# Performance work log

Hardware: AMD Instinct MI355X
Metric: run time of the kernel (lower is better)

Reference implementation:

```python
import jax, jax.numpy as jnp
import numpy as np

N_NEIGHBORS = 15
N_BATCHES = 3
TEMPERATURE = 1.0
DISTANCE_MASK_SENTINEL = 1e10  # pushes self-distance out of the neighborhood
EPS = 1e-8


def setup_inputs() -> dict:
    key = jax.random.key(0)
    k1, k2 = jax.random.split(key)
    embeddings = jax.random.normal(k1, (8192, 512), dtype=jnp.float32)
    batch_labels = jax.random.randint(k2, (8192,), 0, N_BATCHES, dtype=jnp.int32)
    return {"embeddings": embeddings, "batch_labels": batch_labels}


def reference(embeddings, batch_labels):
    n_cells = embeddings.shape[0]
    # pairwise squared euclidean distances: [n, n]
    sq_norms = jnp.sum(embeddings ** 2, axis=-1)
    distances = sq_norms[:, None] + sq_norms[None, :] - 2.0 * (embeddings @ embeddings.T)
    distances = distances + jnp.eye(n_cells, dtype=distances.dtype) * DISTANCE_MASK_SENTINEL

    # soft neighbor weights
    neighbor_weights = jax.nn.softmax(-distances / TEMPERATURE, axis=-1)

    # differentiable sort along rows (jnp.sort is piecewise-linear, differentiable)
    sorted_dists = jnp.sort(distances, axis=-1)
    kth_dist = sorted_dists[:, N_NEIGHBORS - 1:N_NEIGHBORS]  # [n, 1]

    # soft less(distances, kth_dist): sigmoid((kth - d) / softness)
    k_mask = jax.nn.sigmoid((kth_dist - distances) / TEMPERATURE)

    neighbor_weights = neighbor_weights * k_mask
    neighbor_weights = neighbor_weights / (neighbor_weights.sum(axis=-1, keepdims=True) + EPS)

    # batch distribution in each soft neighborhood: [n, n_batches]
    batch_onehot = jax.nn.one_hot(batch_labels, N_BATCHES, dtype=neighbor_weights.dtype)
    batch_dist = neighbor_weights @ batch_onehot

    per_cell_entropy = -jnp.sum(batch_dist * jnp.log(batch_dist + EPS), axis=-1)
    max_entropy = jnp.log(jnp.asarray(N_BATCHES, dtype=jnp.float32))
    normalized_entropy = per_cell_entropy / (max_entropy + EPS)
    return -jnp.mean(normalized_entropy)
```

## Files before the change

### kernel.cpp

```cpp
#include <hip/hip_runtime.h>
#include <math.h>

#define N_CELLS 8192
#define DIM 512
#define TILE 128
#define BK 64
#define KITERS (DIM / BK)
#define NSTRIPE (N_CELLS / TILE)
#define NTRI (NSTRIPE * (NSTRIPE + 1) / 2)
#define SAMPLE 512
#define CAP 512
#define WQCAP 1024

typedef float f32x4 __attribute__((ext_vector_type(4)));
typedef _Float16 f16x8 __attribute__((ext_vector_type(8)));

#define AS1U(p) ((const __attribute__((address_space(1))) unsigned int*)(p))
#define AS3U(p) ((__attribute__((address_space(3))) unsigned int*)(p))

__device__ __forceinline__ unsigned fkey(float f) {
    unsigned u = __float_as_uint(f);
    return (u & 0x80000000u) ? ~u : (u | 0x80000000u);
}
__device__ __forceinline__ float finv(unsigned k) {
    unsigned u = (k & 0x80000000u) ? (k ^ 0x80000000u) : ~k;
    return __uint_as_float(u);
}

__global__ __launch_bounds__(256) void prep_kernel(const float* __restrict__ E,
                                                   unsigned short* __restrict__ Efp,
                                                   float* __restrict__ norms,
                                                   float* __restrict__ out) {
    if (blockIdx.x == 0 && threadIdx.x == 0) out[0] = 0.0f;
    const int wave = threadIdx.x >> 6, lane = threadIdx.x & 63;
    const int row = blockIdx.x * 4 + wave;
    const float4* e4 = (const float4*)(E + (size_t)row * DIM);
    float4 a = e4[lane * 2], b = e4[lane * 2 + 1];
    f16x8 h;
    h[0] = (_Float16)a.x; h[1] = (_Float16)a.y; h[2] = (_Float16)a.z; h[3] = (_Float16)a.w;
    h[4] = (_Float16)b.x; h[5] = (_Float16)b.y; h[6] = (_Float16)b.z; h[7] = (_Float16)b.w;
    const int kc = lane >> 3;
    const int u  = lane & 7;
    *(f16x8*)(Efp + ((size_t)kc * N_CELLS + row) * 64 + (size_t)(u ^ (row & 7)) * 8) = h;
    float s = a.x*a.x + a.y*a.y + a.z*a.z + a.w*a.w
            + b.x*b.x + b.y*b.y + b.z*b.z + b.w*b.w;
    #pragma unroll
    for (int off = 32; off > 0; off >>= 1) s += __shfl_down(s, off, 64);
    if (lane == 0) norms[row] = s;
}

__global__ __launch_bounds__(256) void norms_kernel(const float* __restrict__ E,
                                                    float* __restrict__ norms,
                                                    float* __restrict__ out) {
    if (blockIdx.x == 0 && threadIdx.x == 0) out[0] = 0.0f;
    const int wave = threadIdx.x >> 6, lane = threadIdx.x & 63;
    const int row = blockIdx.x * 4 + wave;
    const float4* e4 = (const float4*)(E + (size_t)row * DIM);
    float4 a = e4[lane], b = e4[lane + 64];
    float s = a.x*a.x + a.y*a.y + a.z*a.z + a.w*a.w
            + b.x*b.x + b.y*b.y + b.z*b.z + b.w*b.w;
    #pragma unroll
    for (int off = 32; off > 0; off >>= 1) s += __shfl_down(s, off, 64);
    if (lane == 0) norms[row] = s;
}


#define STAGE_PACKED(BUF, it)                                                                     \
    do {                                                                                          \
        const unsigned short* pa_ = Efp + ((size_t)(it) * N_CELLS + arow) * 64;                   \
        const unsigned short* pb_ = Efp + ((size_t)(it) * N_CELLS + brow) * 64;                   \
        _Pragma("unroll")                                                                         \
        for (int q_ = 0; q_ < 4; q_++) {                                                          \
            __builtin_amdgcn_global_load_lds(AS1U(pa_ + q_*2048 + t*8),                           \
                                             AS3U((BUF) + q_*4096 + t*16), 16, 0, 0);             \
            __builtin_amdgcn_global_load_lds(AS1U(pb_ + q_*2048 + t*8),                           \
                                             AS3U((BUF) + 16384 + q_*4096 + t*16), 16, 0, 0);     \
        }                                                                                         \
    } while (0)

#define GEMM_COMPUTE(BUF)                                                                         \
    do {                                                                                          \
        _Pragma("unroll")                                                                         \
        for (int ks = 0; ks < 2; ks++) {                                                          \
            f16x8 af[4], bf[4];                                                                   \
            _Pragma("unroll")                                                                     \
            for (int tm = 0; tm < 4; tm++)                                                        \
                af[tm] = *(const f16x8*)((BUF) + (size_t)(wr*64 + tm*16 + fr) * 128               \
                                              + (((ks*4 + kg) * 16) ^ fx));                       \
            _Pragma("unroll")                                                                     \
            for (int tn = 0; tn < 4; tn++)                                                        \
                bf[tn] = *(const f16x8*)((BUF) + 16384 + (size_t)(wc*64 + tn*16 + fr) * 128       \
                                              + (((ks*4 + kg) * 16) ^ fx));                       \
            _Pragma("unroll")                                                                     \
            for (int tm = 0; tm < 4; tm++)                                                        \
                _Pragma("unroll")                                                                 \
                for (int tn = 0; tn < 4; tn++)                                                    \
                    acc[tm][tn] = __builtin_amdgcn_mfma_f32_16x16x32_f16(af[tm], bf[tn],          \
                                                                         acc[tm][tn], 0, 0, 0);  \
        }                                                                                         \
    } while (0)

#define GEMM_LOOP()                                                                               \
    do {                                                                                          \
        _Pragma("unroll")                                                                         \
        for (int it2 = 0; it2 < KITERS; it2 += 2) {                                               \
            __syncthreads();                                                                      \
            STAGE_PACKED(smem, it2);                                                              \
            STAGE_PACKED(smem + 32768, it2 + 1);                                                  \
            __syncthreads();                                                                      \
            GEMM_COMPUTE(smem);                                                                   \
            GEMM_COMPUTE(smem + 32768);                                                           \
        }                                                                                         \
        __syncthreads();                                                                          \
    } while (0)

__global__ __launch_bounds__(256) void samp_dist_kernel(const unsigned short* __restrict__ Efp,
                                                        const float* __restrict__ norms,
                                                        float* __restrict__ Dsamp) {
    __shared__ __align__(16) char smem[65536];

    const int t = threadIdx.x;
    const int lane = t & 63;
    const int w = t >> 6;
    const int wr = w >> 1, wc = w & 1;

    const int arow = blockIdx.y * TILE;
    const int brow = blockIdx.x * TILE;

    const int kg = lane >> 4;
    const int fr = lane & 15;
    const int fx = (fr & 7) << 4;

    f32x4 acc[4][4];
    #pragma unroll
    for (int a = 0; a < 4; a++)
        #pragma unroll
        for (int b = 0; b < 4; b++)
            acc[a][b] = (f32x4){0.f, 0.f, 0.f, 0.f};

    GEMM_LOOP();

    const int colb = brow + wc * 64 + fr;
    const int rowb = arow + wr * 64 + (lane >> 4) * 4;
    #pragma unroll
    for (int tn = 0; tn < 4; tn++) {
        const int col = colb + tn * 16;
        const float nj = norms[col];
        #pragma unroll
        for (int tm = 0; tm < 4; tm++) {
            #pragma unroll
            for (int r = 0; r < 4; r++) {
                const int row = rowb + tm * 16 + r;
                float d = norms[row] + nj - 2.0f * acc[tm][tn][r];
                if (row == col) d += 1e10f;
                Dsamp[(size_t)row * SAMPLE + col] = d;
            }
        }
    }
}

__global__ __launch_bounds__(256) void tsel_kernel(const float* __restrict__ Dsamp,
                                                   float* __restrict__ T,
                                                   int* __restrict__ cnt) {
    const int row = blockIdx.x * 4 + (threadIdx.x >> 6);
    const int lane = threadIdx.x & 63;
    const float4* r4 = (const float4*)(Dsamp + (size_t)row * SAMPLE);

    float v[8];
    #pragma unroll
    for (int s = 0; s < 2; s++) {
        float4 d4 = r4[s * 64 + lane];
        v[s*4+0] = d4.x; v[s*4+1] = d4.y; v[s*4+2] = d4.z; v[s*4+3] = d4.w;
    }
    float mn = v[0], mx = v[0];
    #pragma unroll
    for (int k = 1; k < 8; k++) { mn = fminf(mn, v[k]); mx = fmaxf(mx, v[k]); }
    #pragma unroll
    for (int off = 32; off > 0; off >>= 1) {
        mn = fminf(mn, __shfl_down(mn, off, 64));
        mx = fmaxf(mx, __shfl_down(mx, off, 64));
    }
    mn = __shfl(mn, 0, 64);
    mx = __shfl(mx, 0, 64);

    unsigned lo = fkey(mn), hi = fkey(mx);
    int it = 0;
    while (lo < hi && it < 34) {
        it++;
        const unsigned mid = lo + ((hi - lo) >> 1);
        const float fm = finv(mid);
        int c = 0;
        #pragma unroll
        for (int k = 0; k < 8; k++) c += (v[k] <= fm) ? 1 : 0;
        #pragma unroll
        for (int off = 32; off > 0; off >>= 1) c += __shfl_down(c, off, 64);
        c = __shfl(c, 0, 64);
        if (c >= 15) hi = mid; else lo = mid + 1;
    }
    if (lane == 0) { T[row] = finv(lo); cnt[row] = 0; }
}

__global__ __launch_bounds__(256) void main_cand_kernel(const unsigned short* __restrict__ Efp,
                                                        const float* __restrict__ norms,
                                                        const int* __restrict__ labels,
                                                        const float* __restrict__ T,
                                                        int* __restrict__ cnt,
                                                        int2* __restrict__ cand) {
    __shared__ __align__(16) char smem[65536];

    const int t = threadIdx.x;
    const int lane = t & 63;
    const int w = t >> 6;
    const int wr = w >> 1, wc = w & 1;

    const int fid = blockIdx.x;
    const int y = fid / 65;
    const int x = fid - y * 65;
    const int a = (x <= y) ? y : (NSTRIPE - 1 - y);
    const int b = (x <= y) ? x : (x - y - 1);

    const int arow = a * TILE;
    const int brow = b * TILE;
    const bool diag = (a == b);

    const int kg = lane >> 4;
    const int fr = lane & 15;
    const int fx = (fr & 7) << 4;

    f32x4 acc[4][4];
    #pragma unroll
    for (int aa = 0; aa < 4; aa++)
        #pragma unroll
        for (int bb = 0; bb < 4; bb++)
            acc[aa][bb] = (f32x4){0.f, 0.f, 0.f, 0.f};

    GEMM_LOOP();

    int2* wq = (int2*)(smem + (size_t)w * 8192);

    const int colb = brow + wc * 64 + fr;
    const int rowb = arow + wr * 64 + (lane >> 4) * 4;

    float Trow[4][4], Nrow[4][4];
    int Lrow[4][4];
    #pragma unroll
    for (int tm = 0; tm < 4; tm++)
        #pragma unroll
        for (int r = 0; r < 4; r++) {
            const int row = rowb + tm * 16 + r;
            Trow[tm][r] = T[row];
            Nrow[tm][r] = norms[row];
            Lrow[tm][r] = labels[row];
        }
    float Tcol[4];
    #pragma unroll
    for (int tn = 0; tn < 4; tn++) Tcol[tn] = T[colb + tn * 16];

    int wn = 0;
    #pragma unroll
    for (int tn = 0; tn < 4; tn++) {
        const int col = colb + tn * 16;
        const float nj = norms[col];
        const int labc = labels[col];
        #pragma unroll
        for (int tm = 0; tm < 4; tm++) {
            #pragma unroll
            for (int r = 0; r < 4; r++) {
                const int row = rowb + tm * 16 + r;
                const float d = Nrow[tm][r] + nj - 2.0f * acc[tm][tn][r];
                const bool live = !diag || (row > col);
                {
                    const bool hit = live && (d <= Trow[tm][r]);
                    const unsigned long long bal = __ballot(hit);
                    if (hit) {
                        const int pos = __popcll(bal & ((1ull << lane) - 1ull));
                        if (wn + pos < WQCAP)
                            wq[wn + pos] = make_int2(__float_as_int(d), row | (labc << 13));
                    }
                    wn += (int)__popcll(bal);
                }
                {
                    const bool hit = live && (d <= Tcol[tn]);
                    const unsigned long long bal = __ballot(hit);
                    if (hit) {
                        const int pos = __popcll(bal & ((1ull << lane) - 1ull));
                        if (wn + pos < WQCAP)
                            wq[wn + pos] = make_int2(__float_as_int(d), col | (Lrow[tm][r] << 13));
                    }
                    wn += (int)__popcll(bal);
                }
            }
        }
    }

    const int qn = (wn < WQCAP) ? wn : WQCAP;
    for (int i = lane; i < qn; i += 64) {
        const int2 e = wq[i];
        const int row = e.y & 8191;
        const int lab = e.y >> 13;
        const int idx = atomicAdd(&cnt[row], 1);
        if (idx < CAP) cand[(size_t)row * CAP + idx] = make_int2(e.x, lab);
    }
    if (wn > WQCAP)
        for (int r2 = lane; r2 < TILE; r2 += 64) {
            atomicAdd(&cnt[arow + r2], 1000000);
            atomicAdd(&cnt[brow + r2], 1000000);
        }
}

__global__ __launch_bounds__(256) void final_kernel(const int2* __restrict__ cand,
                                                    const int* __restrict__ cnt,
                                                    const float* __restrict__ T,
                                                    float* __restrict__ rowloss) {
    const int row = blockIdx.x * 4 + (threadIdx.x >> 6);
    const int lane = threadIdx.x & 63;
    const int n = cnt[row];
    if (n < 15 || n > CAP) return;

    float d[CAP / 64];
    int lb[CAP / 64];
    #pragma unroll
    for (int s = 0; s < CAP / 64; s++) {
        const int idx = s * 64 + lane;
        if (idx < n) {
            const int2 c = cand[(size_t)row * CAP + idx];
            d[s] = __int_as_float(c.x);
            lb[s] = c.y;
        } else { d[s] = 3.0e38f; lb[s] = 3; }
    }

    float dmin = d[0];
    #pragma unroll
    for (int s = 1; s < CAP / 64; s++) dmin = fminf(dmin, d[s]);
    #pragma unroll
    for (int off = 32; off > 0; off >>= 1) dmin = fminf(dmin, __shfl_down(dmin, off, 64));
    dmin = __shfl(dmin, 0, 64);

    unsigned lo = fkey(dmin), hi = fkey(T[row]);
    int it = 0;
    while (lo < hi && it < 34) {
        it++;
        const unsigned mid = lo + ((hi - lo) >> 1);
        const float fm = finv(mid);
        int c = 0;
        #pragma unroll
        for (int s = 0; s < CAP / 64; s++) c += (d[s] <= fm) ? 1 : 0;
        #pragma unroll
        for (int off = 32; off > 0; off >>= 1) c += __shfl_down(c, off, 64);
        c = __shfl(c, 0, 64);
        if (c >= 15) hi = mid; else lo = mid + 1;
    }
    const float kth = finv(lo);

    float z = 0.f, s0 = 0.f, s1 = 0.f, s2 = 0.f;
    #pragma unroll
    for (int s = 0; s < CAP / 64; s++) {
        const float w = __expf(dmin - d[s]);
        const float msk = 1.0f / (1.0f + __expf(d[s] - kth));
        const float p = w * msk;
        z  += w;
        s0 += (lb[s] == 0) ? p : 0.f;
        s1 += (lb[s] == 1) ? p : 0.f;
        s2 += (lb[s] == 2) ? p : 0.f;
    }
    #pragma unroll
    for (int off = 32; off > 0; off >>= 1) {
        z  += __shfl_down(z,  off, 64);
        s0 += __shfl_down(s0, off, 64);
        s1 += __shfl_down(s1, off, 64);
        s2 += __shfl_down(s2, off, 64);
    }
    if (lane == 0) {
        const float ssum = s0 + s1 + s2;
        const float denom = ssum + 1e-8f * z;
        const float q0 = s0/denom, q1 = s1/denom, q2 = s2/denom;
        const float H = -(q0*logf(q0+1e-8f) + q1*logf(q1+1e-8f) + q2*logf(q2+1e-8f));
        rowloss[row] = -(H / (logf(3.0f) + 1e-8f)) * (1.0f / N_CELLS);
    }
}

__global__ __launch_bounds__(512) void reduce_kernel(const float* __restrict__ rowloss,
                                                     float* __restrict__ out) {
    __shared__ float wsum[8];
    const int t = threadIdx.x, lane = t & 63, wv = t >> 6;
    const float4* r4 = (const float4*)rowloss;
    float s = 0.f;
    for (int i = t; i < N_CELLS / 4; i += 512) {
        const float4 v = r4[i];
        s += v.x + v.y + v.z + v.w;
    }
    #pragma unroll
    for (int off = 32; off > 0; off >>= 1) s += __shfl_down(s, off, 64);
    if (lane == 0) wsum[wv] = s;
    __syncthreads();
    if (t == 0) {
        float tot = 0.f;
        #pragma unroll
        for (int i = 0; i < 8; i++) tot += wsum[i];
        out[0] = tot;
    }
}

template<int NT>
__device__ __forceinline__ void finish_row(const float* rowb,
                                           float lst[15],
                                           const int* __restrict__ labels,
                                           float* __restrict__ out,
                                           float* __restrict__ rowloss,
                                           int rowidx) {
    constexpr int WAVES = NT / 64;
    __shared__ float w0s[WAVES], w14s[WAVES];
    __shared__ int cnt;
    __shared__ float zz[WAVES], r0s[WAVES], r1s[WAVES], r2s[WAVES];

    const int t = threadIdx.x;
    const int lane = t & 63, wave = t >> 6;

    float m0 = lst[0], m14 = lst[14];
    #pragma unroll
    for (int off = 32; off > 0; off >>= 1) {
        m0  = fminf(m0,  __shfl_down(m0,  off, 64));
        m14 = fminf(m14, __shfl_down(m14, off, 64));
    }
    if (lane == 0) { w0s[wave] = m0; w14s[wave] = m14; }
    __syncthreads();
    float dmin = w0s[0], ub = w14s[0];
    #pragma unroll
    for (int i = 1; i < WAVES; i++) { dmin = fminf(dmin, w0s[i]); ub = fminf(ub, w14s[i]); }

    unsigned lo = fkey(dmin), hi = fkey(ub);
    int iter = 0;
    while (lo < hi && iter < 34) {
        iter++;
        const unsigned mid = lo + ((hi - lo) >> 1);
        const float fmid = finv(mid);
        int c = 0;
        #pragma unroll
        for (int k = 0; k < 15; k++) c += (lst[k] <= fmid) ? 1 : 0;
        #pragma unroll
        for (int off = 32; off > 0; off >>= 1) c += __shfl_down(c, off, 64);
        __syncthreads();
        if (t == 0) cnt = 0;
        __syncthreads();
        if (lane == 0) atomicAdd(&cnt, c);
        __syncthreads();
        const int total = cnt;
        if (total >= 15) hi = mid; else lo = mid + 1;
    }
    const float kth = finv(hi);

    const float4* rb4 = (const float4*)rowb;
    const int4* lb4 = (const int4*)labels;
    float z = 0.f, s0 = 0.f, s1 = 0.f, s2 = 0.f;
    #pragma unroll
    for (int s = 0; s < N_CELLS / (4 * NT); s++) {
        const int idx = s * NT + t;
        const float4 d4 = rb4[idx];
        const int4 l4 = lb4[idx];
        #pragma unroll
        for (int c2 = 0; c2 < 4; c2++) {
            const float d = (c2 == 0) ? d4.x : (c2 == 1) ? d4.y : (c2 == 2) ? d4.z : d4.w;
            const int lab = (c2 == 0) ? l4.x : (c2 == 1) ? l4.y : (c2 == 2) ? l4.z : l4.w;
            const float w = __expf(dmin - d);
            const float msk = 1.0f / (1.0f + __expf(d - kth));
            const float p = w * msk;
            z  += w;
            s0 += (lab == 0) ? p : 0.f;
            s1 += (lab == 1) ? p : 0.f;
            s2 += (lab == 2) ? p : 0.f;
        }
    }
    #pragma unroll
    for (int off = 32; off > 0; off >>= 1) {
        z  += __shfl_down(z,  off, 64);
        s0 += __shfl_down(s0, off, 64);
        s1 += __shfl_down(s1, off, 64);
        s2 += __shfl_down(s2, off, 64);
    }
    if (lane == 0) { zz[wave] = z; r0s[wave] = s0; r1s[wave] = s1; r2s[wave] = s2; }
    __syncthreads();
    if (t == 0) {
        float Z = 0.f, S0 = 0.f, S1 = 0.f, S2 = 0.f;
        #pragma unroll
        for (int i = 0; i < WAVES; i++) { Z += zz[i]; S0 += r0s[i]; S1 += r1s[i]; S2 += r2s[i]; }
        const float ssum = S0 + S1 + S2;
        const float denom = ssum + 1e-8f * Z;
        const float q0 = S0/denom, q1 = S1/denom, q2 = S2/denom;
        const float H = -(q0*logf(q0+1e-8f) + q1*logf(q1+1e-8f) + q2*logf(q2+1e-8f));
        const float contrib = -(H / (logf(3.0f) + 1e-8f)) * (1.0f / N_CELLS);
        if (rowloss) rowloss[rowidx] = contrib;
        else atomicAdd(out, contrib);
    }
}

__device__ void process_row(int i,
                            const float* __restrict__ E,
                            const float* __restrict__ norms,
                            const int* __restrict__ labels,
                            float* __restrict__ out,
                            float* __restrict__ rowloss,
                            float* rowb, float* ei) {
    const int t = threadIdx.x;
    __syncthreads();
    for (int k = t; k < DIM; k += 512) ei[k] = E[(size_t)i * DIM + k];
    __syncthreads();
    const float ni = norms[i];

    float lst[15];
    #pragma unroll
    for (int k = 0; k < 15; k++) lst[k] = 3.0e38f;

    for (int s = 0; s < N_CELLS / 512; s++) {
        const int j = s * 512 + t;
        const float* ej = E + (size_t)j * DIM;
        float dot = 0.f;
        #pragma unroll 4
        for (int k = 0; k < DIM; k += 4) {
            float4 e4 = *(const float4*)(ej + k);
            dot += ei[k]*e4.x + ei[k+1]*e4.y + ei[k+2]*e4.z + ei[k+3]*e4.w;
        }
        float d = ni + norms[j] - 2.0f * dot;
        if (j == i) d += 1e10f;
        rowb[j] = d;
        float v = d;
        #pragma unroll
        for (int k = 0; k < 15; k++) {
            float lo2 = fminf(lst[k], v);
            v = fmaxf(lst[k], v);
            lst[k] = lo2;
        }
    }
    finish_row<512>(rowb, lst, labels, out, rowloss, i);
}

__global__ __launch_bounds__(512) void fused_kernel(const float* __restrict__ E,
                                                    const float* __restrict__ norms,
                                                    const int* __restrict__ labels,
                                                    float* __restrict__ out,
                                                    float* __restrict__ rowloss,
                                                    const int* __restrict__ cnt_g) {
    __shared__ float rowb[N_CELLS];
    __shared__ float ei[DIM];
    __shared__ int bad[TILE];
    __shared__ int nbad;
    const int t = threadIdx.x;

    if (cnt_g == nullptr) {
        process_row(blockIdx.x, E, norms, labels, out, nullptr, rowb, ei);
        return;
    }
    if (t == 0) nbad = 0;
    __syncthreads();
    if (t < TILE) {
        const int row = blockIdx.x * TILE + t;
        const int n = cnt_g[row];
        if (n < 15 || n > CAP) bad[atomicAdd(&nbad, 1)] = row;
    }
    __syncthreads();
    const int nb = nbad;
    for (int b = 0; b < nb; b++)
        process_row(bad[b], E, norms, labels, out, rowloss, rowb, ei);
}

extern "C" void kernel_launch(void* const* d_in, const int* in_sizes, int n_in,
                              void* d_out, int out_size, void* d_ws, size_t ws_size,
                              hipStream_t stream) {
    const float* E = (const float*)d_in[0];
    const int* labels = (const int*)d_in[1];
    float* out = (float*)d_out;

    char* p = (char*)d_ws;
    float* norms = (float*)p;                 p += 32768;
    unsigned short* Efp = (unsigned short*)p; p += (size_t)N_CELLS * DIM * 2;
    float* T = (float*)p;                     p += 32768;
    int* cnt = (int*)p;                       p += 32768;
    float* rowloss = (float*)p;               p += 32768;
    float* Dsamp = (float*)p;                 p += (size_t)N_CELLS * SAMPLE * 4;
    int2* cand = (int2*)p;                    p += (size_t)N_CELLS * CAP * 8;
    const size_t need = (size_t)(p - (char*)d_ws);

    if (ws_size >= need) {
        prep_kernel<<<N_CELLS / 4, 256, 0, stream>>>(E, Efp, norms, out);
        samp_dist_kernel<<<dim3(SAMPLE / TILE, N_CELLS / TILE), 256, 0, stream>>>(Efp, norms, Dsamp);
        tsel_kernel<<<N_CELLS / 4, 256, 0, stream>>>(Dsamp, T, cnt);
        main_cand_kernel<<<NTRI, 256, 0, stream>>>(Efp, norms, labels, T, cnt, cand);
        final_kernel<<<N_CELLS / 4, 256, 0, stream>>>(cand, cnt, T, rowloss);
        fused_kernel<<<N_CELLS / TILE, 512, 0, stream>>>(E, norms, labels, out, rowloss, cnt);
        reduce_kernel<<<1, 512, 0, stream>>>(rowloss, out);
    } else {
        norms_kernel<<<N_CELLS / 4, 256, 0, stream>>>(E, norms, out);
        fused_kernel<<<N_CELLS, 512, 0, stream>>>(E, norms, labels, out, nullptr, nullptr);
    }
}
```

Before: 292.4 us.

## Enlarge threshold sample, shrink candidate cap, fold final reduction into final kernel

The threshold-sampling set doubles (SAMPLE 512→1024) so the per-row top-k threshold T is tighter, which lets the candidate buffer shrink (CAP 512→384) and cuts candidate writes and reads. The separate reduce kernel is removed: final_kernel now does a last-block-done atomic reduction into the output and runs after fused_kernel. The cost is a larger sample distance GEMM and selection, and more rows may overflow CAP and fall back to the slow fused path.

```diff
diff --git a/kernel.cpp b/kernel.cpp
--- a/kernel.cpp
+++ b/kernel.cpp
@@ -8,8 +8,8 @@
 #define KITERS (DIM / BK)
 #define NSTRIPE (N_CELLS / TILE)
 #define NTRI (NSTRIPE * (NSTRIPE + 1) / 2)
-#define SAMPLE 512
-#define CAP 512
+#define SAMPLE 1024
+#define CAP 384
 #define WQCAP 1024
 
 typedef float f32x4 __attribute__((ext_vector_type(4)));
@@ -30,8 +30,9 @@
 __global__ __launch_bounds__(256) void prep_kernel(const float* __restrict__ E,
                                                    unsigned short* __restrict__ Efp,
                                                    float* __restrict__ norms,
-                                                   float* __restrict__ out) {
-    if (blockIdx.x == 0 && threadIdx.x == 0) out[0] = 0.0f;
+                                                   float* __restrict__ out,
+                                                   unsigned* __restrict__ done) {
+    if (blockIdx.x == 0 && threadIdx.x == 0) { out[0] = 0.0f; done[0] = 0u; }
     const int wave = threadIdx.x >> 6, lane = threadIdx.x & 63;
     const int row = blockIdx.x * 4 + wave;
     const float4* e4 = (const float4*)(E + (size_t)row * DIM);
@@ -166,15 +167,15 @@
     const int lane = threadIdx.x & 63;
     const float4* r4 = (const float4*)(Dsamp + (size_t)row * SAMPLE);
 
-    float v[8];
-    #pragma unroll
-    for (int s = 0; s < 2; s++) {
+    float v[16];
+    #pragma unroll
+    for (int s = 0; s < 4; s++) {
         float4 d4 = r4[s * 64 + lane];
         v[s*4+0] = d4.x; v[s*4+1] = d4.y; v[s*4+2] = d4.z; v[s*4+3] = d4.w;
     }
     float mn = v[0], mx = v[0];
     #pragma unroll
-    for (int k = 1; k < 8; k++) { mn = fminf(mn, v[k]); mx = fmaxf(mx, v[k]); }
+    for (int k = 1; k < 16; k++) { mn = fminf(mn, v[k]); mx = fmaxf(mx, v[k]); }
     #pragma unroll
     for (int off = 32; off > 0; off >>= 1) {
         mn = fminf(mn, __shfl_down(mn, off, 64));
@@ -191,7 +192,7 @@
         const float fm = finv(mid);
         int c = 0;
         #pragma unroll
-        for (int k = 0; k < 8; k++) c += (v[k] <= fm) ? 1 : 0;
+        for (int k = 0; k < 16; k++) c += (v[k] <= fm) ? 1 : 0;
         #pragma unroll
         for (int off = 32; off > 0; off >>= 1) c += __shfl_down(c, off, 64);
         c = __shfl(c, 0, 64);
@@ -311,93 +312,100 @@
 __global__ __launch_bounds__(256) void final_kernel(const int2* __restrict__ cand,
                                                     const int* __restrict__ cnt,
                                                     const float* __restrict__ T,
-                                                    float* __restrict__ rowloss) {
+                                                    float* __restrict__ rowloss,
+                                                    float* __restrict__ out,
+                                                    unsigned* __restrict__ done) {
+    __shared__ bool isLast;
+    __shared__ float wsum[4];
     const int row = blockIdx.x * 4 + (threadIdx.x >> 6);
     const int lane = threadIdx.x & 63;
+    const int wv = threadIdx.x >> 6;
     const int n = cnt[row];
-    if (n < 15 || n > CAP) return;
-
-    float d[CAP / 64];
-    int lb[CAP / 64];
-    #pragma unroll
-    for (int s = 0; s < CAP / 64; s++) {
-        const int idx = s * 64 + lane;
-        if (idx < n) {
-            const int2 c = cand[(size_t)row * CAP + idx];
-            d[s] = __int_as_float(c.x);
-            lb[s] = c.y;
-        } else { d[s] = 3.0e38f; lb[s] = 3; }
-    }
-
-    float dmin = d[0];
-    #pragma unroll
-    for (int s = 1; s < CAP / 64; s++) dmin = fminf(dmin, d[s]);
-    #pragma unroll
-    for (int off = 32; off > 0; off >>= 1) dmin = fminf(dmin, __shfl_down(dmin, off, 64));
-    dmin = __shfl(dmin, 0, 64);
-
-    unsigned lo = fkey(dmin), hi = fkey(T[row]);
-    int it = 0;
-    while (lo < hi && it < 34) {
-        it++;
-        const unsigned mid = lo + ((hi - lo) >> 1);
-        const float fm = finv(mid);
-        int c = 0;
-        #pragma unroll
-        for (int s = 0; s < CAP / 64; s++) c += (d[s] <= fm) ? 1 : 0;
-        #pragma unroll
-        for (int off = 32; off > 0; off >>= 1) c += __shfl_down(c, off, 64);
-        c = __shfl(c, 0, 64);
-        if (c >= 15) hi = mid; else lo = mid + 1;
-    }
-    const float kth = finv(lo);
-
-    float z = 0.f, s0 = 0.f, s1 = 0.f, s2 = 0.f;
-    #pragma unroll
-    for (int s = 0; s < CAP / 64; s++) {
-        const float w = __expf(dmin - d[s]);
-        const float msk = 1.0f / (1.0f + __expf(d[s] - kth));
-        const float p = w * msk;
-        z  += w;
-        s0 += (lb[s] == 0) ? p : 0.f;
-        s1 += (lb[s] == 1) ? p : 0.f;
-        s2 += (lb[s] == 2) ? p : 0.f;
-    }
-    #pragma unroll
-    for (int off = 32; off > 0; off >>= 1) {
-        z  += __shfl_down(z,  off, 64);
-        s0 += __shfl_down(s0, off, 64);
-        s1 += __shfl_down(s1, off, 64);
-        s2 += __shfl_down(s2, off, 64);
-    }
-    if (lane == 0) {
-        const float ssum = s0 + s1 + s2;
-        const float denom = ssum + 1e-8f * z;
-        const float q0 = s0/denom, q1 = s1/denom, q2 = s2/denom;
-        const float H = -(q0*logf(q0+1e-8f) + q1*logf(q1+1e-8f) + q2*logf(q2+1e-8f));
-        rowloss[row] = -(H / (logf(3.0f) + 1e-8f)) * (1.0f / N_CELLS);
-    }
-}
-
-__global__ __launch_bounds__(512) void reduce_kernel(const float* __restrict__ rowloss,
-                                                     float* __restrict__ out) {
-    __shared__ float wsum[8];
-    const int t = threadIdx.x, lane = t & 63, wv = t >> 6;
-    const float4* r4 = (const float4*)rowloss;
-    float s = 0.f;
-    for (int i = t; i < N_CELLS / 4; i += 512) {
-        const float4 v = r4[i];
-        s += v.x + v.y + v.z + v.w;
-    }
-    #pragma unroll
-    for (int off = 32; off > 0; off >>= 1) s += __shfl_down(s, off, 64);
-    if (lane == 0) wsum[wv] = s;
-    __syncthreads();
-    if (t == 0) {
-        float tot = 0.f;
-        #pragma unroll
-        for (int i = 0; i < 8; i++) tot += wsum[i];
-        out[0] = tot;
+
+    if (n >= 15 && n <= CAP) {
+        float d[CAP / 64];
+        int lb[CAP / 64];
+        #pragma unroll
+        for (int s = 0; s < CAP / 64; s++) {
+            const int idx = s * 64 + lane;
+            if (idx < n) {
+                const int2 c = cand[(size_t)row * CAP + idx];
+                d[s] = __int_as_float(c.x);
+                lb[s] = c.y;
+            } else { d[s] = 3.0e38f; lb[s] = 3; }
+        }
+
+        float dmin = d[0];
+        #pragma unroll
+        for (int s = 1; s < CAP / 64; s++) dmin = fminf(dmin, d[s]);
+        #pragma unroll
+        for (int off = 32; off > 0; off >>= 1) dmin = fminf(dmin, __shfl_down(dmin, off, 64));
+        dmin = __shfl(dmin, 0, 64);
+
+        unsigned lo = fkey(dmin), hi = fkey(T[row]);
+        int it = 0;
+        while (lo < hi && it < 34) {
+            it++;
+            const unsigned mid = lo + ((hi - lo) >> 1);
+            const float fm = finv(mid);
+            int c = 0;
+            #pragma unroll
+            for (int s = 0; s < CAP / 64; s++) c += (d[s] <= fm) ? 1 : 0;
+            #pragma unroll
+            for (int off = 32; off > 0; off >>= 1) c += __shfl_down(c, off, 64);
+            c = __shfl(c, 0, 64);
+            if (c >= 15) hi = mid; else lo = mid + 1;
+        }
+        const float kth = finv(lo);
+
+        float z = 0.f, s0 = 0.f, s1 = 0.f, s2 = 0.f;
+        #pragma unroll
+        for (int s = 0; s < CAP / 64; s++) {
+            const float w = __expf(dmin - d[s]);
+            const float msk = 1.0f / (1.0f + __expf(d[s] - kth));
+            const float p = w * msk;
+            z  += w;
+            s0 += (lb[s] == 0) ? p : 0.f;
+            s1 += (lb[s] == 1) ? p : 0.f;
+            s2 += (lb[s] == 2) ? p : 0.f;
+        }
+        #pragma unroll
+        for (int off = 32; off > 0; off >>= 1) {
+            z  += __shfl_down(z,  off, 64);
+            s0 += __shfl_down(s0, off, 64);
+            s1 += __shfl_down(s1, off, 64);
+            s2 += __shfl_down(s2, off, 64);
+        }
+        if (lane == 0) {
+            const float ssum = s0 + s1 + s2;
+            const float denom = ssum + 1e-8f * z;
+            const float q0 = s0/denom, q1 = s1/denom, q2 = s2/denom;
+            const float H = -(q0*logf(q0+1e-8f) + q1*logf(q1+1e-8f) + q2*logf(q2+1e-8f));
+            rowloss[row] = -(H / (logf(3.0f) + 1e-8f)) * (1.0f / N_CELLS);
+        }
+    }
+
+    __threadfence();
+    __syncthreads();
+    if (threadIdx.x == 0) {
+        const unsigned r = atomicAdd(done, 1u);
+        isLast = (r == (unsigned)(gridDim.x - 1));
+    }
+    __syncthreads();
+    if (isLast) {
+        __threadfence();
+        const float4* r4 = (const float4*)rowloss;
+        float s = 0.f;
+        for (int i = threadIdx.x; i < N_CELLS / 4; i += 256) {
+            const float4 v = r4[i];
+            s += v.x + v.y + v.z + v.w;
+        }
+        #pragma unroll
+        for (int off = 32; off > 0; off >>= 1) s += __shfl_down(s, off, 64);
+        if (lane == 0) wsum[wv] = s;
+        __syncthreads();
+        if (threadIdx.x == 0)
+            out[0] = wsum[0] + wsum[1] + wsum[2] + wsum[3];
     }
 }
 
@@ -575,18 +583,18 @@
     float* T = (float*)p;                     p += 32768;
     int* cnt = (int*)p;                       p += 32768;
     float* rowloss = (float*)p;               p += 32768;
+    unsigned* done = (unsigned*)p;            p += 4096;
     float* Dsamp = (float*)p;                 p += (size_t)N_CELLS * SAMPLE * 4;
     int2* cand = (int2*)p;                    p += (size_t)N_CELLS * CAP * 8;
     const size_t need = (size_t)(p - (char*)d_ws);
 
     if (ws_size >= need) {
-        prep_kernel<<<N_CELLS / 4, 256, 0, stream>>>(E, Efp, norms, out);
+        prep_kernel<<<N_CELLS / 4, 256, 0, stream>>>(E, Efp, norms, out, done);
         samp_dist_kernel<<<dim3(SAMPLE / TILE, N_CELLS / TILE), 256, 0, stream>>>(Efp, norms, Dsamp);
         tsel_kernel<<<N_CELLS / 4, 256, 0, stream>>>(Dsamp, T, cnt);
         main_cand_kernel<<<NTRI, 256, 0, stream>>>(Efp, norms, labels, T, cnt, cand);
-        final_kernel<<<N_CELLS / 4, 256, 0, stream>>>(cand, cnt, T, rowloss);
         fused_kernel<<<N_CELLS / TILE, 512, 0, stream>>>(E, norms, labels, out, rowloss, cnt);
-        reduce_kernel<<<1, 512, 0, stream>>>(rowloss, out);
+        final_kernel<<<N_CELLS / 4, 256, 0, stream>>>(cand, cnt, T, rowloss, out, done);
     } else {
         norms_kernel<<<N_CELLS / 4, 256, 0, stream>>>(E, norms, out);
         fused_kernel<<<N_CELLS, 512, 0, stream>>>(E, norms, labels, out, nullptr, nullptr);
```

Measured after the change: 369.5 us. 1.26x slower.
